# Kernel optimization log

Hardware: AMD Instinct MI355X
Metric: run time of the kernel (lower is better)

The kernel has to match this reference:

```python
import jax, jax.numpy as jnp
import numpy as np

NUM_HEADS = 16
HEAD_DIM = 64
TOP_K_TILES = 8
TILE_SIZE = 16
ROPE_BASE = 10000.0


def make_freqs_cis(seq_len, head_dim):
    # [seq, head_dim//2] complex64, standard RoPE frequencies
    inv_freq = 1.0 / (ROPE_BASE ** (jnp.arange(0, head_dim, 2, dtype=jnp.float32) / head_dim))
    angles = jnp.arange(seq_len, dtype=jnp.float32)[:, None] * inv_freq[None, :]
    return jax.lax.complex(jnp.cos(angles), jnp.sin(angles))


def apply_rope(xq, xk, freqs_cis):
    # xq, xk: [b, h, s, d]; pairs adjacent channels as (real, imag)
    xq_ = xq.astype(jnp.float32).reshape(*xq.shape[:-1], -1, 2)
    xk_ = xk.astype(jnp.float32).reshape(*xk.shape[:-1], -1, 2)
    xq_c = jax.lax.complex(xq_[..., 0], xq_[..., 1])
    xk_c = jax.lax.complex(xk_[..., 0], xk_[..., 1])
    f = freqs_cis[None, None, :xq.shape[2], :]
    xq_r = xq_c * f
    xk_r = xk_c * f
    xq_out = jnp.stack([xq_r.real, xq_r.imag], axis=-1).reshape(xq.shape)
    xk_out = jnp.stack([xk_r.real, xk_r.imag], axis=-1).reshape(xk.shape)
    return xq_out.astype(xq.dtype), xk_out.astype(xk.dtype)


def setup_inputs() -> dict:
    key = jax.random.key(0)
    ks = jax.random.split(key, 5)
    B, S, D = 2, 2048, 1024
    scale = 1.0 / np.sqrt(D)
    return {
        "x": jax.random.normal(ks[0], (B, S, D), dtype=jnp.float32),
        "wq": jax.random.normal(ks[1], (D, NUM_HEADS * HEAD_DIM), dtype=jnp.float32) * scale,
        "wk": jax.random.normal(ks[2], (D, NUM_HEADS * HEAD_DIM), dtype=jnp.float32) * scale,
        "wv": jax.random.normal(ks[3], (D, NUM_HEADS * HEAD_DIM), dtype=jnp.float32) * scale,
        "wo": jax.random.normal(ks[4], (NUM_HEADS * HEAD_DIM, D), dtype=jnp.float32) * scale,
    }


def reference(x, wq, wk, wv, wo):
    batch, seq_len, _ = x.shape
    q = (x @ wq).reshape(batch, seq_len, NUM_HEADS, HEAD_DIM)
    k = (x @ wk).reshape(batch, seq_len, NUM_HEADS, HEAD_DIM)
    v = (x @ wv).reshape(batch, seq_len, NUM_HEADS, HEAD_DIM)

    freqs_cis = make_freqs_cis(seq_len, HEAD_DIM)
    q_t = jnp.transpose(q, (0, 2, 1, 3))
    k_t = jnp.transpose(k, (0, 2, 1, 3))
    q_t, k_t = apply_rope(q_t, k_t, freqs_cis)
    q = jnp.transpose(q_t, (0, 2, 1, 3))
    k = jnp.transpose(k_t, (0, 2, 1, 3))

    logits = jnp.einsum('bqhd,bkhd->bhqk', q, k) / jnp.sqrt(jnp.float32(HEAD_DIM))
    causal = jnp.tril(jnp.ones((seq_len, seq_len), dtype=bool))
    logits = jnp.where(causal[None, None, :, :], logits, -1e10)
    weights = jax.nn.softmax(logits, axis=-1)  # [b, h, q, k]

    # Scout: tile-max-pool last token's attention probs + top-k tile selection
    last_token_probs = weights[:, :, -1, :]  # [b, h, k]
    pad_len = (TILE_SIZE - seq_len % TILE_SIZE) % TILE_SIZE
    if pad_len > 0:
        last_token_probs = jnp.pad(last_token_probs, ((0, 0), (0, 0), (0, pad_len)))
    num_tiles = last_token_probs.shape[-1] // TILE_SIZE
    tile_scores = jnp.max(
        last_token_probs.reshape(batch, NUM_HEADS, num_tiles, TILE_SIZE), axis=-1)
    _, top_tile_indices = jax.lax.top_k(tile_scores, TOP_K_TILES)  # [b, h, top_k]

    output = jnp.einsum('bhqk,bkhd->bqhd', weights, v)
    output = output.reshape(batch, seq_len, NUM_HEADS * HEAD_DIM)
    output = output @ wo
    return output, top_tile_indices
```

## Files before the change

### kernel.cpp

```cpp
#include <hip/hip_runtime.h>

#define B_ 2
#define S_ 2048
#define E_ 1024
#define H_ 16
#define D_ 64
#define BS_ (B_*S_)
#define PSTR 76

typedef unsigned short u16;
typedef __attribute__((ext_vector_type(8))) short short8;
typedef __attribute__((ext_vector_type(4))) float floatx4;
typedef __bf16 bf16x8 __attribute__((ext_vector_type(8)));

__device__ __forceinline__ u16 f2bf(float f) {
    unsigned int u = __builtin_bit_cast(unsigned int, f);
    u += 0x7FFFu + ((u >> 16) & 1u);
    return (u16)(u >> 16);
}
__device__ __forceinline__ float bf2f(u16 h) {
    return __builtin_bit_cast(float, (unsigned int)h << 16);
}
__device__ __forceinline__ floatx4 mfma16(short8 a, short8 b, floatx4 c) {
    return __builtin_amdgcn_mfma_f32_16x16x32_bf16(
        __builtin_bit_cast(bf16x8, a), __builtin_bit_cast(bf16x8, b), c, 0, 0, 0);
}
__device__ __forceinline__ void gload_lds16(const void* g, void* l) {
    __builtin_amdgcn_global_load_lds(
        (const __attribute__((address_space(1))) unsigned int*)g,
        (__attribute__((address_space(3))) unsigned int*)l, 16, 0, 0);
}


__global__ __launch_bounds__(256) void rope_table_kernel(float* __restrict__ cost,
                                                         float* __restrict__ sint) {
    int idx = blockIdx.x * 256 + threadIdx.x;
    int s = idx >> 5, i = idx & 31;
    float inv = powf(10000.0f, -(float)i / 32.0f);
    float a = (float)s * inv;
    cost[idx] = cosf(a);
    sint[idx] = sinf(a);
}

__global__ __launch_bounds__(256) void convert_x_kernel(const float* __restrict__ X,
                                                        u16* __restrict__ xcat) {
    int i = blockIdx.x * 256 + threadIdx.x;
    int row = i >> 8, c4 = (i & 255) * 4;
    float4 v = ((const float4*)X)[i];
    u16 h0 = f2bf(v.x), h1 = f2bf(v.y), h2 = f2bf(v.z), h3 = f2bf(v.w);
    uint2 o;
    o.x = (unsigned)h0 | ((unsigned)h1 << 16);
    o.y = (unsigned)h2 | ((unsigned)h3 << 16);
    *(uint2*)&xcat[(size_t)row * 2048 + c4] = o;
    u16 l0 = f2bf(v.x - bf2f(h0)), l1 = f2bf(v.y - bf2f(h1));
    u16 l2 = f2bf(v.z - bf2f(h2)), l3 = f2bf(v.w - bf2f(h3));
    uint2 ol;
    ol.x = (unsigned)l0 | ((unsigned)l1 << 16);
    ol.y = (unsigned)l2 | ((unsigned)l3 << 16);
    *(uint2*)&xcat[(size_t)row * 2048 + 1024 + c4] = ol;
}

__global__ __launch_bounds__(256) void transpose_w4_kernel(const float* __restrict__ wq,
                                                           const float* __restrict__ wk,
                                                           const float* __restrict__ wv,
                                                           const float* __restrict__ wo,
                                                           u16* __restrict__ wqt,
                                                           u16* __restrict__ wkt,
                                                           u16* __restrict__ wkres,
                                                           u16* __restrict__ wvt,
                                                           u16* __restrict__ wot) {
    __shared__ float t[32][33];
    int bx = blockIdx.x;
    int which = bx >> 10, sub = bx & 1023;
    const float* W = which == 0 ? wq : which == 1 ? wk : which == 2 ? wv : wo;
    u16* Wt = which == 0 ? wqt : which == 1 ? wkt : which == 2 ? wvt : wot;
    int tk = (sub >> 5) * 32, tn = (sub & 31) * 32;
    int tx = threadIdx.x & 31, ty = threadIdx.x >> 5;
    for (int i = 0; i < 32; i += 8)
        t[ty + i][tx] = W[(size_t)(tk + ty + i) * E_ + tn + tx];
    __syncthreads();
    for (int i = 0; i < 32; i += 8) {
        float v = t[tx][ty + i];
        u16 hi = f2bf(v);
        Wt[(size_t)(tn + ty + i) * E_ + tk + tx] = hi;
        if (which == 1) {
            wkres[(size_t)(tn + ty + i) * 2048 + tk + tx] = f2bf(v - bf2f(hi));
            wkres[(size_t)(tn + ty + i) * 2048 + 1024 + tk + tx] = hi;
        }
    }
}


__device__ __forceinline__ void stage_swz(const u16* __restrict__ src, int row0, int k0,
                                          int stride, u16* lds, int tid) {
    int wv = tid >> 6, ln = tid & 63;
    int swz = (((ln & 7) ^ (ln >> 3)) << 3);
    int rr = ln >> 3;
#pragma unroll
    for (int i = 0; i < 4; ++i) {
        int seg = i * 4 + wv;
        gload_lds16(&src[(size_t)(row0 + seg * 8 + rr) * stride + k0 + swz],
                    (char*)lds + (size_t)seg * 1024);
    }
}

__device__ __forceinline__ void gemm_body(const u16* lA, const u16* lB,
                                          floatx4 (*acc)[4], int lane, int wave) {
    int wm = (wave >> 1) * 64, wn = (wave & 1) * 64;
    int lr = lane & 15, lq = lane >> 4, r7 = lr & 7;
#pragma unroll
    for (int half = 0; half < 2; ++half) {
        int xo = (((half * 4 + lq) ^ r7) << 3);
        short8 afr[4], bfr[4];
#pragma unroll
        for (int mi = 0; mi < 4; ++mi)
            afr[mi] = *(const short8*)&lA[(wm + mi * 16 + lr) * 64 + xo];
#pragma unroll
        for (int ni = 0; ni < 4; ++ni)
            bfr[ni] = *(const short8*)&lB[(wn + ni * 16 + lr) * 64 + xo];
        __builtin_amdgcn_s_setprio(1);
#pragma unroll
        for (int mi = 0; mi < 4; ++mi)
#pragma unroll
            for (int ni = 0; ni < 4; ++ni)
                acc[mi][ni] = mfma16(afr[mi], bfr[ni], acc[mi][ni]);
        __builtin_amdgcn_s_setprio(0);
    }
}

__device__ __forceinline__ void gemm_write(float* __restrict__ C, floatx4 (*acc)[4],
                                           int m0, int n0, int N, int lane, int wave) {
    int wm = (wave >> 1) * 64, wn = (wave & 1) * 64;
    int lr = lane & 15, lq = lane >> 4;
#pragma unroll
    for (int mi = 0; mi < 4; ++mi)
#pragma unroll
        for (int ni = 0; ni < 4; ++ni)
#pragma unroll
            for (int r = 0; r < 4; ++r)
                C[(size_t)(m0 + wm + mi * 16 + lq * 4 + r) * N + n0 + wn + ni * 16 + lr]
                    = acc[mi][ni][r];
}

__device__ __forceinline__ void rope_epilogue(floatx4 (*acc)[4], int m0, int n0,
                                              const float* __restrict__ cost,
                                              const float* __restrict__ sint,
                                              u16* __restrict__ dstb,
                                              float* __restrict__ dstf,
                                              int lane, int wave) {
    int wm = (wave >> 1) * 64, wn = (wave & 1) * 64;
    int lr = lane & 15, lq = lane >> 4;
    int odd = lr & 1;
    int h = (n0 + wn) >> 6;
#pragma unroll
    for (int ni = 0; ni < 4; ++ni) {
        int d = ni * 16 + lr;
        int i = d >> 1;
#pragma unroll
        for (int mi = 0; mi < 4; ++mi) {
#pragma unroll
            for (int r = 0; r < 4; ++r) {
                int row = m0 + wm + mi * 16 + lq * 4 + r;
                int s = row & 2047, bq = row >> 11;
                float own = acc[mi][ni][r];
                float par = __shfl_xor(own, 1);
                float e = odd ? par : own;
                float o = odd ? own : par;
                float c = cost[s * 32 + i], sn = sint[s * 32 + i];
                float out = odd ? (e * sn + o * c) : (e * c - o * sn);
                size_t off = (((size_t)(bq * 16 + h)) * S_ + s) * 64 + d;
                dstb[off] = f2bf(out);
                if (dstf) dstf[off] = out;
            }
        }
    }
}

__device__ __forceinline__ void v_epilogue(floatx4 (*acc)[4], int m0, int n0,
                                           u16* vt, u16* __restrict__ vtb,
                                           int lane, int wave, int tid) {
    int wm = (wave >> 1) * 64, wn = (wave & 1) * 64;
    int lr = lane & 15, lq = lane >> 4;
#pragma unroll
    for (int ni = 0; ni < 4; ++ni) {
        int dcol = wn + ni * 16 + lr;
#pragma unroll
        for (int mi = 0; mi < 4; ++mi)
#pragma unroll
            for (int r = 0; r < 4; ++r)
                vt[dcol * 136 + wm + mi * 16 + lq * 4 + r] = f2bf(acc[mi][ni][r]);
    }
    __syncthreads();
    int dcol = tid >> 1, sh = (tid & 1) * 64;
    int colg = n0 + dcol, h = colg >> 6, d = colg & 63;
    int bq = m0 >> 11, s0 = m0 & 2047;
    size_t base = (((size_t)(bq * 16 + h)) * 64 + d) * S_ + s0 + sh;
#pragma unroll
    for (int c = 0; c < 8; ++c)
        *(uint4*)&vtb[base + c * 8] = *(const uint4*)&vt[dcol * 136 + sh + c * 8];
}

__global__ __launch_bounds__(256) void proj_gemm_kernel(const u16* __restrict__ xcat,
                                                        const u16* __restrict__ wqt,
                                                        const u16* __restrict__ wkt,
                                                        const u16* __restrict__ wkres,
                                                        const u16* __restrict__ wvt,
                                                        const float* __restrict__ cost,
                                                        const float* __restrict__ sint,
                                                        u16* __restrict__ qb,
                                                        u16* __restrict__ kb,
                                                        float* __restrict__ klogf,
                                                        u16* __restrict__ vtb) {
    __shared__ __align__(16) u16 lsbuf[17408];
    u16* lA = lsbuf;
    u16* lB = lsbuf + 8192;
    int bx = blockIdx.x;
    int role = bx >> 8;
    int idx = bx & 255;
    int m0 = (idx >> 3) * 128, n0 = (idx & 7) * 128;
    int tid = threadIdx.x, lane = tid & 63, wave = tid >> 6;

    floatx4 acc[4][4];
#pragma unroll
    for (int i = 0; i < 4; ++i)
#pragma unroll
        for (int j = 0; j < 4; ++j) acc[i][j] = (floatx4){0.f, 0.f, 0.f, 0.f};

    if (role == 0) {
        for (int k0 = 0; k0 < 1024; k0 += 64) {
            stage_swz(xcat, m0, k0, 2048, lA, tid);
            stage_swz(wkt, n0, k0, 1024, lB, tid);
            __syncthreads();
            gemm_body(lA, lB, acc, lane, wave);
            __syncthreads();
        }
        for (int k0 = 0; k0 < 2048; k0 += 64) {
            stage_swz(xcat, m0, k0, 2048, lA, tid);
            stage_swz(wkres, n0, k0, 2048, lB, tid);
            __syncthreads();
            gemm_body(lA, lB, acc, lane, wave);
            __syncthreads();
        }
        rope_epilogue(acc, m0, n0, cost, sint, kb, klogf, lane, wave);
    } else if (role == 1) {
        for (int k0 = 0; k0 < 1024; k0 += 64) {
            stage_swz(xcat, m0, k0, 2048, lA, tid);
            stage_swz(wqt, n0, k0, 1024, lB, tid);
            __syncthreads();
            gemm_body(lA, lB, acc, lane, wave);
            __syncthreads();
        }
        rope_epilogue(acc, m0, n0, cost, sint, qb, (float*)nullptr, lane, wave);
    } else {
        for (int k0 = 0; k0 < 1024; k0 += 64) {
            stage_swz(xcat, m0, k0, 2048, lA, tid);
            stage_swz(wvt, n0, k0, 1024, lB, tid);
            __syncthreads();
            gemm_body(lA, lB, acc, lane, wave);
            __syncthreads();
        }
        v_epilogue(acc, m0, n0, lsbuf, vtb, lane, wave, tid);
    }
}

__global__ __launch_bounds__(256) void gemm_bf16_kernel(const u16* __restrict__ A,
                                                        const u16* __restrict__ Bt,
                                                        float* __restrict__ C,
                                                        int M, int N, int Kd) {
    __shared__ __align__(16) u16 lA[128 * 64];
    __shared__ __align__(16) u16 lB[128 * 64];
    int nwg = (M / 128) * (N / 128);
    int bx = blockIdx.x;
    int q = nwg >> 3, rr = nwg & 7, xcd = bx & 7, pos = bx >> 3;
    int lbx = (xcd < rr ? xcd * (q + 1) : rr * (q + 1) + (xcd - rr) * q) + pos;
    int nbn = N / 128;
    int m0 = (lbx / nbn) * 128, n0 = (lbx % nbn) * 128;
    int tid = threadIdx.x, lane = tid & 63, wave = tid >> 6;

    floatx4 acc[4][4];
#pragma unroll
    for (int i = 0; i < 4; ++i)
#pragma unroll
        for (int j = 0; j < 4; ++j) acc[i][j] = (floatx4){0.f, 0.f, 0.f, 0.f};

    for (int k0 = 0; k0 < Kd; k0 += 64) {
        stage_swz(A, m0, k0, Kd, lA, tid);
        stage_swz(Bt, n0, k0, Kd, lB, tid);
        __syncthreads();
        gemm_body(lA, lB, acc, lane, wave);
        __syncthreads();
    }
    gemm_write(C, acc, m0, n0, N, lane, wave);
}

__global__ __launch_bounds__(256) void qlast_kernel(const float* __restrict__ x,
                                                    const float* __restrict__ wq,
                                                    float* __restrict__ qlast) {
    __shared__ float red[8][32];
    int bx = blockIdx.x;
    int b = bx >> 5, c0 = (bx & 31) * 32;
    int cl = threadIdx.x & 31, kc = threadIdx.x >> 5;
    const float* xr = &x[((size_t)b * S_ + (S_ - 1)) * E_ + kc * 128];
    const float* wp = &wq[(size_t)(kc * 128) * E_ + c0 + cl];
    float acc = 0.f;
#pragma unroll 4
    for (int e = 0; e < 128; ++e) acc = fmaf(xr[e], wp[(size_t)e * E_], acc);
    red[kc][cl] = acc;
    __syncthreads();
    if (kc == 0) {
        float s = ((red[0][cl] + red[1][cl]) + (red[2][cl] + red[3][cl]))
                + ((red[4][cl] + red[5][cl]) + (red[6][cl] + red[7][cl]));
        qlast[(size_t)b * E_ + c0 + cl] = s;
    }
}

__device__ __forceinline__ void stage_kv(const u16* __restrict__ K, const u16* __restrict__ V,
                                         int n0, u16* kbuf, u16* vbuf, int wave, int lane) {
    int lr = lane & 15, lq = lane >> 4;
    if (wave < 2) {
#pragma unroll
        for (int i = 0; i < 4; ++i) {
            int sk = wave * 4 + i;
            int kt = sk >> 1, kh = (sk & 1) * 32;
            gload_lds16(&K[(size_t)(n0 + kt * 16 + lr) * D_ + kh + lq * 8],
                        kbuf + sk * 512);
        }
    } else {
#pragma unroll
        for (int i = 0; i < 4; ++i) {
            int sv = (wave - 2) * 4 + i;
            int c = sv >> 2, o = sv & 3;
            gload_lds16(&V[(size_t)(o * 16 + lr) * S_ + n0 + c * 32 + lq * 8],
                        vbuf + sv * 512);
        }
    }
}

__global__ __launch_bounds__(256) void flash_kernel(const u16* __restrict__ qb,
                                                    const u16* __restrict__ kb,
                                                    const u16* __restrict__ vtb,
                                                    u16* __restrict__ ab) {
    __shared__ __align__(16) u16 kls[2][8 * 512];
    __shared__ __align__(16) u16 vls[2][8 * 512];
    __shared__ __align__(16) u16 ldsP[4][16 * PSTR];
    int tid = threadIdx.x;
    int lane = tid & 63, wave = tid >> 6;
    int bx = blockIdx.x;
    int xcd = bx & 7, ii = bx >> 3;
    int hid = xcd + 8 * (ii & 3);
    int qc = 31 - (ii >> 2);
    int qt0 = qc * 64 + wave * 16;
    const u16* Q = qb + (size_t)hid * S_ * D_;
    const u16* K = kb + (size_t)hid * S_ * D_;
    const u16* V = vtb + (size_t)hid * D_ * S_;
    u16* lp = &ldsP[wave][0];
    int lr = lane & 15, lq = lane >> 4, lk = lq * 8;

    short8 qfr0 = *(const short8*)&Q[(size_t)(qt0 + lr) * D_ + lk];
    short8 qfr1 = *(const short8*)&Q[(size_t)(qt0 + lr) * D_ + 32 + lk];

    floatx4 o0 = {0,0,0,0}, o1 = {0,0,0,0}, o2 = {0,0,0,0}, o3 = {0,0,0,0};
    float m = -1e30f, l = 0.f;

    stage_kv(K, V, 0, kls[0], vls[0], wave, lane);
    asm volatile("s_waitcnt vmcnt(0)" ::: "memory");
    __syncthreads();

    for (int it = 0; it <= qc; ++it) {
        int n0 = it * 64;
        int buf = it & 1;
        const u16* kbuf = kls[buf];
        const u16* vbuf = vls[buf];
        if (it < qc)
            stage_kv(K, V, n0 + 64, kls[buf ^ 1], vls[buf ^ 1], wave, lane);

        short8 ka0[4], ka1[4];
#pragma unroll
        for (int kt = 0; kt < 4; ++kt) {
            ka0[kt] = *(const short8*)&kbuf[(kt * 2 + 0) * 512 + lane * 8];
            ka1[kt] = *(const short8*)&kbuf[(kt * 2 + 1) * 512 + lane * 8];
        }
        floatx4 st[4];
#pragma unroll
        for (int kt = 0; kt < 4; ++kt) st[kt] = (floatx4){0.f, 0.f, 0.f, 0.f};
        __builtin_amdgcn_s_setprio(1);
#pragma unroll
        for (int kt = 0; kt < 4; ++kt) {
            st[kt] = mfma16(ka0[kt], qfr0, st[kt]);
            st[kt] = mfma16(ka1[kt], qfr1, st[kt]);
        }
        __builtin_amdgcn_s_setprio(0);

        const float SC = 0.18033688011112042f;
        int rem = qt0 + 16 - n0;
        float sv[4][4];
        float bmax = -1e30f;
        if (rem >= 80) {
#pragma unroll
            for (int kt = 0; kt < 4; ++kt)
#pragma unroll
                for (int r = 0; r < 4; ++r) {
                    float s = st[kt][r] * SC;
                    sv[kt][r] = s;
                    bmax = fmaxf(bmax, s);
                }
        } else {
#pragma unroll
            for (int kt = 0; kt < 4; ++kt)
#pragma unroll
                for (int r = 0; r < 4; ++r) {
                    int k = n0 + kt * 16 + lq * 4 + r;
                    float s = (k <= qt0 + lr) ? st[kt][r] * SC : -1e30f;
                    sv[kt][r] = s;
                    bmax = fmaxf(bmax, s);
                }
        }
        bmax = fmaxf(bmax, __shfl_xor(bmax, 16));
        bmax = fmaxf(bmax, __shfl_xor(bmax, 32));
        if (!__all(bmax <= m + 8.0f)) {
            float mn = fmaxf(m, bmax);
            float alpha = __builtin_amdgcn_exp2f(m - mn);
            m = mn;
            l *= alpha;
            float af[4];
#pragma unroll
            for (int r = 0; r < 4; ++r) af[r] = __shfl(alpha, lq * 4 + r);
#pragma unroll
            for (int r = 0; r < 4; ++r) {
                o0[r] *= af[r]; o1[r] *= af[r]; o2[r] *= af[r]; o3[r] *= af[r];
            }
        }
        float ps = 0.f;
#pragma unroll
        for (int kt = 0; kt < 4; ++kt) {
            float p0 = __builtin_amdgcn_exp2f(sv[kt][0] - m);
            float p1 = __builtin_amdgcn_exp2f(sv[kt][1] - m);
            float p2 = __builtin_amdgcn_exp2f(sv[kt][2] - m);
            float p3 = __builtin_amdgcn_exp2f(sv[kt][3] - m);
            ps += (p0 + p1) + (p2 + p3);
            unsigned wlo, whi;
            asm("v_cvt_pk_bf16_f32 %0, %1, %2" : "=v"(wlo) : "v"(p0), "v"(p1));
            asm("v_cvt_pk_bf16_f32 %0, %1, %2" : "=v"(whi) : "v"(p2), "v"(p3));
            *(uint2*)&lp[lr * PSTR + kt * 16 + lq * 4] = (uint2){wlo, whi};
        }
        ps += __shfl_xor(ps, 16);
        ps += __shfl_xor(ps, 32);
        l += ps;

        short8 vv[2][4];
#pragma unroll
        for (int c = 0; c < 2; ++c)
#pragma unroll
            for (int o = 0; o < 4; ++o)
                vv[c][o] = *(const short8*)&vbuf[(c * 4 + o) * 512 + lane * 8];
        asm volatile("s_waitcnt lgkmcnt(0)" ::: "memory");
        __builtin_amdgcn_s_setprio(1);
#pragma unroll
        for (int c = 0; c < 2; ++c) {
            uint2 plo = *(const uint2*)&lp[lr * PSTR + c * 32 + lk];
            uint2 phi = *(const uint2*)&lp[lr * PSTR + c * 32 + lk + 4];
            short8 pfr = __builtin_bit_cast(short8, (uint4){plo.x, plo.y, phi.x, phi.y});
            o0 = mfma16(pfr, vv[c][0], o0);
            o1 = mfma16(pfr, vv[c][1], o1);
            o2 = mfma16(pfr, vv[c][2], o2);
            o3 = mfma16(pfr, vv[c][3], o3);
        }
        __builtin_amdgcn_s_setprio(0);

        if (it < qc) {
            asm volatile("s_waitcnt vmcnt(0)" ::: "memory");
            __syncthreads();
        }
    }
    float li[4];
#pragma unroll
    for (int r = 0; r < 4; ++r) li[r] = 1.0f / __shfl(l, lq * 4 + r);
    int b = hid >> 4, h = hid & 15;
    size_t orow_base = ((size_t)b * S_ + qt0 + lq * 4) * E_ + h * D_;
#pragma unroll
    for (int r = 0; r < 4; ++r) {
        size_t rb = orow_base + (size_t)r * E_;
        ab[rb + 0  + lr] = f2bf(o0[r] * li[r]);
        ab[rb + 16 + lr] = f2bf(o1[r] * li[r]);
        ab[rb + 32 + lr] = f2bf(o2[r] * li[r]);
        ab[rb + 48 + lr] = f2bf(o3[r] * li[r]);
    }
}

__global__ __launch_bounds__(256) void topk_scores_kernel(const float* __restrict__ qlast,
                                                          const float* __restrict__ klogf,
                                                          const float* __restrict__ cost,
                                                          const float* __restrict__ sint,
                                                          float* __restrict__ tscores) {
    __shared__ float qr[64];
    __shared__ float lmax[256];
    int bx = blockIdx.x;
    int chunk = bx & 7, bh = bx >> 3;
    int b = bh >> 4, h = bh & 15;
    int tid = threadIdx.x;
    if (tid < 32) {
        float c = cost[2047 * 32 + tid], sn = sint[2047 * 32 + tid];
        float q0 = qlast[(size_t)b * E_ + h * 64 + 2 * tid];
        float q1 = qlast[(size_t)b * E_ + h * 64 + 2 * tid + 1];
        qr[2 * tid]     = q0 * c - q1 * sn;
        qr[2 * tid + 1] = q0 * sn + q1 * c;
    }
    __syncthreads();
    int s = chunk * 256 + tid;
    const float4* kr = (const float4*)&klogf[((size_t)bh * S_ + s) * 64];
    float acc = 0.f;
#pragma unroll
    for (int i = 0; i < 16; ++i) {
        float4 kv = kr[i];
        acc += qr[4*i] * kv.x + qr[4*i+1] * kv.y + qr[4*i+2] * kv.z + qr[4*i+3] * kv.w;
    }
    lmax[tid] = acc;
    __syncthreads();
    if (tid < 16) {
        float mx = lmax[tid * 16];
#pragma unroll
        for (int j = 1; j < 16; ++j) mx = fmaxf(mx, lmax[tid * 16 + j]);
        tscores[bh * 128 + chunk * 16 + tid] = mx;
    }
}

__global__ __launch_bounds__(64) void topk_select_kernel(const float* __restrict__ tscores,
                                                         float* __restrict__ oidx) {
    int bh = blockIdx.x, tid = threadIdx.x;
    float v0 = tscores[bh * 128 + tid], v1 = tscores[bh * 128 + 64 + tid];
    float va, vb; int ia, ib;
    if (v1 > v0) { va = v1; ia = tid + 64; vb = v0; ib = tid; }
    else         { va = v0; ia = tid;      vb = v1; ib = tid + 64; }
    float cv = va; int ci = ia; int used = 0;
    for (int t = 0; t < 8; ++t) {
        float bv = cv; int bi = ci;
#pragma unroll
        for (int mk = 1; mk < 64; mk <<= 1) {
            float ov = __shfl_xor(bv, mk);
            int oi = __shfl_xor(bi, mk);
            if (ov > bv || (ov == bv && oi < bi)) { bv = ov; bi = oi; }
        }
        if (tid == 0) oidx[bh * 8 + t] = (float)bi;
        if (ci == bi) {
            if (used == 0) { cv = vb; ci = ib; used = 1; }
            else           { cv = -3e30f; ci = 1 << 20; }
        }
    }
}

extern "C" void kernel_launch(void* const* d_in, const int* in_sizes, int n_in,
                              void* d_out, int out_size, void* d_ws, size_t ws_size,
                              hipStream_t stream) {
    (void)in_sizes; (void)n_in; (void)out_size; (void)ws_size;
    const float* x  = (const float*)d_in[0];
    const float* wq = (const float*)d_in[1];
    const float* wk = (const float*)d_in[2];
    const float* wv = (const float*)d_in[3];
    const float* wo = (const float*)d_in[4];
    float* out = (float*)d_out;

    char* wsp = (char*)d_ws;
    size_t off = 0;
    auto nxt = [&](size_t bytes) {
        char* p = wsp + off;
        off = (off + bytes + 255) & ~(size_t)255;
        return p;
    };
    u16* xcat  = (u16*)nxt((size_t)BS_ * 2048 * 2);
    u16* wqt   = (u16*)nxt((size_t)E_ * E_ * 2);
    u16* wkt   = (u16*)nxt((size_t)E_ * E_ * 2);
    u16* wkres = (u16*)nxt((size_t)E_ * 2048 * 2);
    u16* wvt   = (u16*)nxt((size_t)E_ * E_ * 2);
    u16* wot   = (u16*)nxt((size_t)E_ * E_ * 2);
    float* cost = (float*)nxt((size_t)S_ * 32 * 4);
    float* sint = (float*)nxt((size_t)S_ * 32 * 4);
    u16* qb    = (u16*)nxt((size_t)B_ * H_ * S_ * D_ * 2);
    u16* kb    = (u16*)nxt((size_t)B_ * H_ * S_ * D_ * 2);
    float* klogf = (float*)nxt((size_t)B_ * H_ * S_ * D_ * 4);
    u16* vtb   = (u16*)nxt((size_t)B_ * H_ * S_ * D_ * 2);
    u16* ab    = (u16*)nxt((size_t)BS_ * E_ * 2);
    float* qlast = (float*)nxt((size_t)B_ * E_ * 4);
    float* tscores = (float*)nxt((size_t)B_ * H_ * 128 * 4);

    hipLaunchKernelGGL(rope_table_kernel, dim3(S_ * 32 / 256), dim3(256), 0, stream, cost, sint);
    hipLaunchKernelGGL(convert_x_kernel, dim3(BS_ * E_ / 4 / 256), dim3(256), 0, stream, x, xcat);
    hipLaunchKernelGGL(transpose_w4_kernel, dim3(4096), dim3(256), 0, stream,
                       wq, wk, wv, wo, wqt, wkt, wkres, wvt, wot);

    hipLaunchKernelGGL(proj_gemm_kernel, dim3(768), dim3(256), 0, stream,
                       xcat, wqt, wkt, wkres, wvt, cost, sint, qb, kb, klogf, vtb);
    hipLaunchKernelGGL(qlast_kernel, dim3(64), dim3(256), 0, stream, x, wq, qlast);

    hipLaunchKernelGGL(flash_kernel, dim3(B_ * H_ * (S_ / 64)), dim3(256), 0, stream,
                       qb, kb, vtb, ab);

    hipLaunchKernelGGL(topk_scores_kernel, dim3(B_ * H_ * 8), dim3(256), 0, stream,
                       qlast, klogf, cost, sint, tscores);
    hipLaunchKernelGGL(topk_select_kernel, dim3(B_ * H_), dim3(64), 0, stream,
                       tscores, out + (size_t)BS_ * E_);

    hipLaunchKernelGGL(gemm_bf16_kernel, dim3(256), dim3(256), 0, stream, ab, wot, out,
                       BS_, E_, E_);
}
```

Measured before the change: 245.8 us.

## Fuse top-k tile scoring into K projection epilogue and remap blocks for XCD locality

The K-projection RoPE epilogue now computes the dot product of each rotated key row with the rotated last-token query and reduces tile maxima in-register, writing tile scores directly. This removes the fp32 K copy (klogf), its global write and re-read, and the separate topk_scores kernel launch. qlast is now computed before the projection GEMM to feed it. The block index mapping is also changed so that blocks which likely share an XCD cover neighbouring M tiles, aiming for better L2 reuse. The cost is extra shuffles and registers in the K epilogue.

```diff
diff --git a/kernel.cpp b/kernel.cpp
--- a/kernel.cpp
+++ b/kernel.cpp
@@ -145,13 +145,33 @@
 __device__ __forceinline__ void rope_epilogue(floatx4 (*acc)[4], int m0, int n0,
                                               const float* __restrict__ cost,
                                               const float* __restrict__ sint,
+                                              const float* __restrict__ qlast,
                                               u16* __restrict__ dstb,
-                                              float* __restrict__ dstf,
+                                              float* __restrict__ tscores,
                                               int lane, int wave) {
     int wm = (wave >> 1) * 64, wn = (wave & 1) * 64;
     int lr = lane & 15, lq = lane >> 4;
     int odd = lr & 1;
     int h = (n0 + wn) >> 6;
+    int bq = m0 >> 11;
+    int s0 = m0 & 2047;
+    float qr[4];
+    if (qlast) {
+#pragma unroll
+        for (int ni = 0; ni < 4; ++ni) {
+            int d = ni * 16 + lr;
+            int i = d >> 1;
+            float qv = qlast[(size_t)bq * E_ + h * 64 + d];
+            float qp = __shfl_xor(qv, 1);
+            float c = cost[2047 * 32 + i], sn = sint[2047 * 32 + i];
+            qr[ni] = odd ? (qp * sn + qv * c) : (qv * c - qp * sn);
+        }
+    }
+    float dotp[4][4];
+#pragma unroll
+    for (int mi = 0; mi < 4; ++mi)
+#pragma unroll
+        for (int r = 0; r < 4; ++r) dotp[mi][r] = 0.f;
 #pragma unroll
     for (int ni = 0; ni < 4; ++ni) {
         int d = ni * 16 + lr;
@@ -161,17 +181,33 @@
 #pragma unroll
             for (int r = 0; r < 4; ++r) {
                 int row = m0 + wm + mi * 16 + lq * 4 + r;
-                int s = row & 2047, bq = row >> 11;
+                int s = row & 2047;
                 float own = acc[mi][ni][r];
                 float par = __shfl_xor(own, 1);
-                float e = odd ? par : own;
-                float o = odd ? own : par;
                 float c = cost[s * 32 + i], sn = sint[s * 32 + i];
-                float out = odd ? (e * sn + o * c) : (e * c - o * sn);
-                size_t off = (((size_t)(bq * 16 + h)) * S_ + s) * 64 + d;
-                dstb[off] = f2bf(out);
-                if (dstf) dstf[off] = out;
+                float out = odd ? (par * sn + own * c) : (own * c - par * sn);
+                dstb[(((size_t)(bq * 16 + h)) * S_ + s) * 64 + d] = f2bf(out);
+                if (qlast) dotp[mi][r] += out * qr[ni];
             }
+        }
+    }
+    if (qlast) {
+#pragma unroll
+        for (int mi = 0; mi < 4; ++mi) {
+            float tm = -1e30f;
+#pragma unroll
+            for (int r = 0; r < 4; ++r) {
+                float dv = dotp[mi][r];
+                dv += __shfl_xor(dv, 1);
+                dv += __shfl_xor(dv, 2);
+                dv += __shfl_xor(dv, 4);
+                dv += __shfl_xor(dv, 8);
+                tm = fmaxf(tm, dv);
+            }
+            tm = fmaxf(tm, __shfl_xor(tm, 16));
+            tm = fmaxf(tm, __shfl_xor(tm, 32));
+            if (lane == 0)
+                tscores[(size_t)(bq * 16 + h) * 128 + (s0 >> 4) + (wm >> 4) + mi] = tm;
         }
     }
 }
@@ -207,9 +243,10 @@
                                                         const u16* __restrict__ wvt,
                                                         const float* __restrict__ cost,
                                                         const float* __restrict__ sint,
+                                                        const float* __restrict__ qlast,
                                                         u16* __restrict__ qb,
                                                         u16* __restrict__ kb,
-                                                        float* __restrict__ klogf,
+                                                        float* __restrict__ tscores,
                                                         u16* __restrict__ vtb) {
     __shared__ __align__(16) u16 lsbuf[17408];
     u16* lA = lsbuf;
@@ -217,7 +254,9 @@
     int bx = blockIdx.x;
     int role = bx >> 8;
     int idx = bx & 255;
-    int m0 = (idx >> 3) * 128, n0 = (idx & 7) * 128;
+    int xcd = idx & 7, loc = idx >> 3;
+    int m0 = (xcd * 4 + (loc & 3)) * 128;
+    int n0 = (loc >> 2) * 128;
     int tid = threadIdx.x, lane = tid & 63, wave = tid >> 6;
 
     floatx4 acc[4][4];
@@ -241,7 +280,7 @@
             gemm_body(lA, lB, acc, lane, wave);
             __syncthreads();
         }
-        rope_epilogue(acc, m0, n0, cost, sint, kb, klogf, lane, wave);
+        rope_epilogue(acc, m0, n0, cost, sint, qlast, kb, tscores, lane, wave);
     } else if (role == 1) {
         for (int k0 = 0; k0 < 1024; k0 += 64) {
             stage_swz(xcat, m0, k0, 2048, lA, tid);
@@ -250,7 +289,8 @@
             gemm_body(lA, lB, acc, lane, wave);
             __syncthreads();
         }
-        rope_epilogue(acc, m0, n0, cost, sint, qb, (float*)nullptr, lane, wave);
+        rope_epilogue(acc, m0, n0, cost, sint, (const float*)nullptr, qb,
+                      (float*)nullptr, lane, wave);
     } else {
         for (int k0 = 0; k0 < 1024; k0 += 64) {
             stage_swz(xcat, m0, k0, 2048, lA, tid);
@@ -487,43 +527,6 @@
     }
 }
 
-__global__ __launch_bounds__(256) void topk_scores_kernel(const float* __restrict__ qlast,
-                                                          const float* __restrict__ klogf,
-                                                          const float* __restrict__ cost,
-                                                          const float* __restrict__ sint,
-                                                          float* __restrict__ tscores) {
-    __shared__ float qr[64];
-    __shared__ float lmax[256];
-    int bx = blockIdx.x;
-    int chunk = bx & 7, bh = bx >> 3;
-    int b = bh >> 4, h = bh & 15;
-    int tid = threadIdx.x;
-    if (tid < 32) {
-        float c = cost[2047 * 32 + tid], sn = sint[2047 * 32 + tid];
-        float q0 = qlast[(size_t)b * E_ + h * 64 + 2 * tid];
-        float q1 = qlast[(size_t)b * E_ + h * 64 + 2 * tid + 1];
-        qr[2 * tid]     = q0 * c - q1 * sn;
-        qr[2 * tid + 1] = q0 * sn + q1 * c;
-    }
-    __syncthreads();
-    int s = chunk * 256 + tid;
-    const float4* kr = (const float4*)&klogf[((size_t)bh * S_ + s) * 64];
-    float acc = 0.f;
-#pragma unroll
-    for (int i = 0; i < 16; ++i) {
-        float4 kv = kr[i];
-        acc += qr[4*i] * kv.x + qr[4*i+1] * kv.y + qr[4*i+2] * kv.z + qr[4*i+3] * kv.w;
-    }
-    lmax[tid] = acc;
-    __syncthreads();
-    if (tid < 16) {
-        float mx = lmax[tid * 16];
-#pragma unroll
-        for (int j = 1; j < 16; ++j) mx = fmaxf(mx, lmax[tid * 16 + j]);
-        tscores[bh * 128 + chunk * 16 + tid] = mx;
-    }
-}
-
 __global__ __launch_bounds__(64) void topk_select_kernel(const float* __restrict__ tscores,
                                                          float* __restrict__ oidx) {
     int bh = blockIdx.x, tid = threadIdx.x;
@@ -576,7 +579,6 @@
     float* sint = (float*)nxt((size_t)S_ * 32 * 4);
     u16* qb    = (u16*)nxt((size_t)B_ * H_ * S_ * D_ * 2);
     u16* kb    = (u16*)nxt((size_t)B_ * H_ * S_ * D_ * 2);
-    float* klogf = (float*)nxt((size_t)B_ * H_ * S_ * D_ * 4);
     u16* vtb   = (u16*)nxt((size_t)B_ * H_ * S_ * D_ * 2);
     u16* ab    = (u16*)nxt((size_t)BS_ * E_ * 2);
     float* qlast = (float*)nxt((size_t)B_ * E_ * 4);
@@ -586,16 +588,15 @@
     hipLaunchKernelGGL(convert_x_kernel, dim3(BS_ * E_ / 4 / 256), dim3(256), 0, stream, x, xcat);
     hipLaunchKernelGGL(transpose_w4_kernel, dim3(4096), dim3(256), 0, stream,
                        wq, wk, wv, wo, wqt, wkt, wkres, wvt, wot);
+    hipLaunchKernelGGL(qlast_kernel, dim3(64), dim3(256), 0, stream, x, wq, qlast);
 
     hipLaunchKernelGGL(proj_gemm_kernel, dim3(768), dim3(256), 0, stream,
-                       xcat, wqt, wkt, wkres, wvt, cost, sint, qb, kb, klogf, vtb);
-    hipLaunchKernelGGL(qlast_kernel, dim3(64), dim3(256), 0, stream, x, wq, qlast);
+                       xcat, wqt, wkt, wkres, wvt, cost, sint, qlast,
+                       qb, kb, tscores, vtb);
 
     hipLaunchKernelGGL(flash_kernel, dim3(B_ * H_ * (S_ / 64)), dim3(256), 0, stream,
                        qb, kb, vtb, ab);
 
-    hipLaunchKernelGGL(topk_scores_kernel, dim3(B_ * H_ * 8), dim3(256), 0, stream,
-                       qlast, klogf, cost, sint, tscores);
     hipLaunchKernelGGL(topk_select_kernel, dim3(B_ * H_), dim3(64), 0, stream,
                        tscores, out + (size_t)BS_ * E_);
 
```

After: 223.2 us. 1.1x faster.
